# Optimization experiments

Measured on AMD Instinct MI355X. Metric: run time of the kernel, lower is better.

Reference implementation:

```python
import jax, jax.numpy as jnp
import numpy as np

B, S, H, P = 8, 2048, 256, 64
NQ = 20

def setup_inputs() -> dict:
    key = jax.random.key(0)
    ks = jax.random.split(key, 12)
    s = lambda fan_in: 1.0 / np.sqrt(fan_in)
    return {
        "feature_x": jax.random.normal(ks[0], (B, S, H), dtype=jnp.float32),
        "param_x": jax.random.normal(ks[1], (B, S, P), dtype=jnp.float32),
        "sim_w1": jax.random.uniform(ks[2], (H, H // 2), jnp.float32, -s(H), s(H)),
        "sim_b1": jax.random.uniform(ks[3], (H // 2,), jnp.float32, -s(H), s(H)),
        "sim_w2": jax.random.uniform(ks[4], (H // 2, 1), jnp.float32, -s(H // 2), s(H // 2)),
        "sim_b2": jax.random.uniform(ks[5], (1,), jnp.float32, -s(H // 2), s(H // 2)),
        "conf_w1": jax.random.uniform(ks[6], (H, H // 2), jnp.float32, -s(H), s(H)),
        "conf_b1": jax.random.uniform(ks[7], (H // 2,), jnp.float32, -s(H), s(H)),
        "conf_w2": jax.random.uniform(ks[8], (H // 2, 1), jnp.float32, -s(H // 2), s(H // 2)),
        "conf_b2": jax.random.uniform(ks[9], (1,), jnp.float32, -s(H // 2), s(H // 2)),
        "questions": jax.random.randint(ks[10], (B, S), 0, NQ, dtype=jnp.int64 if jax.config.jax_enable_x64 else jnp.int32),
    }

def _mlp_scalar(x, w1, b1, w2, b2):
    # [B,S,H] -> [B,S] (dropout is eval-mode identity)
    h = jax.nn.relu(jnp.einsum("bsh,hk->bsk", x, w1) + b1)
    return (jnp.einsum("bsk,ko->bso", h, w2) + b2)[..., 0]

def reference(feature_x, param_x, sim_w1, sim_b1, sim_w2, sim_b2,
              conf_w1, conf_b1, conf_w2, conf_b2, questions):
    similarities = _mlp_scalar(feature_x, sim_w1, sim_b1, sim_w2, sim_b2)          # [B,S]
    confidences = jax.nn.sigmoid(_mlp_scalar(feature_x, conf_w1, conf_b1, conf_w2, conf_b2))  # [B,S]
    # multiplicative equality mask (zeros, not -inf, outside group — faithful to source)
    qmask = (questions[:, :, None] == questions[:, None, :]).astype(feature_x.dtype)  # [B,S,S]
    logits = similarities[:, :, None] * qmask                                        # [B,i,j]
    attn = jax.nn.softmax(logits, axis=-2)                                           # softmax over i
    smoothed = jnp.einsum("bij,bip->bjp", attn, param_x)                              # attn^T @ param_x
    c = confidences[..., None]
    return c * param_x + (1.0 - c) * smoothed
```

## Files before the change

### kernel.cpp

```cpp
#include <hip/hip_runtime.h>
#include <math.h>

#define B_  8
#define S_  2048
#define H_  256
#define HK_ 128
#define P_  64
#define NQ_ 20
#define M_  (B_*S_)
#define ACC_STRIDE 2688
#define NREP 4

#define WS_CONF  0
#define WS_ACC   16384
#define WS_WT    (16384 + NREP*B_*ACC_STRIDE)

typedef __attribute__((ext_vector_type(8))) short bf16x8;
typedef __attribute__((ext_vector_type(4))) float f32x4;

__global__ void prep_kernel(const float* __restrict__ sw1, const float* __restrict__ cw1,
                            short* __restrict__ wtf, float* __restrict__ ws_acc)
{
    const int t = blockIdx.x * 256 + threadIdx.x;
    const int l = t & 63, nt = (t >> 6) & 7, kt = (t >> 9) & 7, mlp = t >> 12;
    const int col = l & 15, quad = l >> 4;
    const int n = nt * 16 + col;
    const float* w1 = mlp ? cw1 : sw1;
    short frag[8];
    #pragma unroll
    for (int j = 0; j < 8; ++j) {
        int k = kt * 32 + quad * 8 + j;
        union { float f; unsigned u; } c; c.f = w1[k * HK_ + n];
        frag[j] = (short)((c.u + 0x7FFF + ((c.u >> 16) & 1)) >> 16);
    }
    *(uint4*)(wtf + (size_t)t * 8) = *(const uint4*)frag;
    for (int s = t; s < NREP * B_ * ACC_STRIDE; s += 8192) ws_acc[s] = 0.f;
}

__launch_bounds__(256)
__global__ void mlp_accum_kernel(const float* __restrict__ fx, const short* __restrict__ wtf,
                                 const float* __restrict__ sb1, const float* __restrict__ sw2,
                                 const float* __restrict__ sb2, const float* __restrict__ cb1,
                                 const float* __restrict__ cw2, const float* __restrict__ cb2,
                                 const float* __restrict__ px, const int* __restrict__ questions,
                                 float* __restrict__ conf, float* __restrict__ ws_acc)
{
    __shared__ float accs[ACC_STRIDE];
    __shared__ float sim_l[32];

    const int tid  = threadIdx.x;
    for (int s = tid; s < ACC_STRIDE; s += 256) accs[s] = 0.f;

    const int w    = tid >> 6, l = tid & 63;
    const int col  = l & 15, quad = l >> 4;
    const int mlp  = w >> 1, mt = w & 1;
    const int row  = blockIdx.x * 32 + mt * 16 + col;

    f32x4 acc[8];
    #pragma unroll
    for (int nt = 0; nt < 8; ++nt) acc[nt] = (f32x4){0.f, 0.f, 0.f, 0.f};

    const float* fxrow = fx + (size_t)row * H_;
    const short* wf = wtf + (size_t)mlp * 32768 + (size_t)l * 8;

    #pragma unroll
    for (int kt = 0; kt < 8; ++kt) {
        float4 a0 = *(const float4*)(fxrow + kt * 32 + quad * 8);
        float4 a1 = *(const float4*)(fxrow + kt * 32 + quad * 8 + 4);
        float af[8] = {a0.x, a0.y, a0.z, a0.w, a1.x, a1.y, a1.z, a1.w};
        bf16x8 ahi, alo;
        #pragma unroll
        for (int i = 0; i < 8; ++i) {
            union { float f; unsigned u; } c; c.f = af[i];
            unsigned hi = c.u >> 16;
            ahi[i] = (short)hi;
            union { float f; unsigned u; } h2; h2.u = hi << 16;
            union { float f; unsigned u; } c2; c2.f = af[i] - h2.f;
            alo[i] = (short)(c2.u >> 16);
        }
        const short* base = wf + (size_t)kt * 4096;
        #pragma unroll
        for (int nt = 0; nt < 8; ++nt) {
            bf16x8 bf = *(const bf16x8*)(base + nt * 512);
            acc[nt] = __builtin_amdgcn_mfma_f32_16x16x32_bf16(ahi, bf, acc[nt], 0, 0, 0);
            acc[nt] = __builtin_amdgcn_mfma_f32_16x16x32_bf16(alo, bf, acc[nt], 0, 0, 0);
        }
    }

    const float* b1 = mlp ? cb1 : sb1;
    const float* w2 = mlp ? cw2 : sw2;
    const float  b2v = mlp ? cb2[0] : sb2[0];
    float p[4] = {0.f, 0.f, 0.f, 0.f};
    #pragma unroll
    for (int nt = 0; nt < 8; ++nt) {
        float b1c = b1[nt * 16 + col];
        float w2c = w2[nt * 16 + col];
        #pragma unroll
        for (int j = 0; j < 4; ++j)
            p[j] += fmaxf(acc[nt][j] + b1c, 0.f) * w2c;
    }
    #pragma unroll
    for (int off = 8; off >= 1; off >>= 1)
        #pragma unroll
        for (int j = 0; j < 4; ++j) p[j] += __shfl_down(p[j], off, 16);

    if (col == 0) {
        #pragma unroll
        for (int j = 0; j < 4; ++j) {
            int rloc = mt * 16 + quad * 4 + j;
            float v = p[j] + b2v;
            if (mlp == 0) sim_l[rloc] = v;
            else          conf[blockIdx.x * 32 + rloc] = 1.0f / (1.0f + expf(-v));
        }
    }
    __syncthreads();

    const int row0 = blockIdx.x * 32;
    float Treg = 0.f;
    #pragma unroll
    for (int t = 0; t < 8; ++t) {
        const int il = w + 4 * t;
        const int i  = row0 + il;
        const int qi = questions[i];
        const float e = expf(sim_l[il]);
        const float v = px[(size_t)i * P_ + l];
        Treg += v;
        atomicAdd(&accs[qi * 64 + l], v);
        atomicAdd(&accs[(20 + qi) * 64 + l], e * v);
        if (l == 0) {
            atomicAdd(&accs[2624 + qi], e);
            atomicAdd(&accs[2644 + qi], 1.0f);
        }
    }
    atomicAdd(&accs[2560 + l], Treg);
    __syncthreads();

    const int b   = blockIdx.x >> 6;
    const int rep = blockIdx.x & (NREP - 1);
    float* dst = ws_acc + (size_t)(b * NREP + rep) * ACC_STRIDE;
    for (int s = tid; s < ACC_STRIDE; s += 256) {
        const float vv = accs[s];
        if (vv != 0.f) atomicAdd(dst + s, vv);
    }
}

__global__ void output_kernel(const float* __restrict__ px, const float* __restrict__ conf,
                              const int* __restrict__ questions, const float* __restrict__ ws_acc,
                              float* __restrict__ out)
{
    const int idx = blockIdx.x * 256 + threadIdx.x;
    const int row = idx >> 4;
    const int p4  = idx & 15;
    const int b   = row >> 11;
    const float c = conf[row];
    const int   q = questions[row];

    float Tx=0.f,Ty=0.f,Tz=0.f,Tw=0.f;
    float Gx=0.f,Gy=0.f,Gz=0.f,Gw=0.f;
    float Ex=0.f,Ey=0.f,Ez=0.f,Ew=0.f;
    float Wq=0.f, nq=0.f;
    #pragma unroll
    for (int rep = 0; rep < NREP; ++rep) {
        const float* a = ws_acc + (size_t)(b * NREP + rep) * ACC_STRIDE;
        const float4 t4 = *(const float4*)(a + 2560 + p4 * 4);
        const float4 g4 = *(const float4*)(a + q * 64 + p4 * 4);
        const float4 e4 = *(const float4*)(a + (20 + q) * 64 + p4 * 4);
        Tx += t4.x; Ty += t4.y; Tz += t4.z; Tw += t4.w;
        Gx += g4.x; Gy += g4.y; Gz += g4.z; Gw += g4.w;
        Ex += e4.x; Ey += e4.y; Ez += e4.z; Ew += e4.w;
        Wq += a[2624 + q]; nq += a[2644 + q];
    }
    const float denom = ((float)S_ - nq) + Wq;
    const float inv = 1.0f / denom;
    const float4 pv = ((const float4*)px)[idx];
    const float om = 1.0f - c;
    float4 o;
    o.x = c * pv.x + om * ((Tx - Gx + Ex) * inv);
    o.y = c * pv.y + om * ((Ty - Gy + Ey) * inv);
    o.z = c * pv.z + om * ((Tz - Gz + Ez) * inv);
    o.w = c * pv.w + om * ((Tw - Gw + Ew) * inv);
    ((float4*)out)[idx] = o;
}

extern "C" void kernel_launch(void* const* d_in, const int* in_sizes, int n_in,
                              void* d_out, int out_size, void* d_ws, size_t ws_size,
                              hipStream_t stream) {
    const float* fx  = (const float*)d_in[0];
    const float* px  = (const float*)d_in[1];
    const float* sw1 = (const float*)d_in[2];
    const float* sb1 = (const float*)d_in[3];
    const float* sw2 = (const float*)d_in[4];
    const float* sb2 = (const float*)d_in[5];
    const float* cw1 = (const float*)d_in[6];
    const float* cb1 = (const float*)d_in[7];
    const float* cw2 = (const float*)d_in[8];
    const float* cb2 = (const float*)d_in[9];
    const int* questions = (const int*)d_in[10];
    float* out = (float*)d_out;

    float* ws     = (float*)d_ws;
    float* conf   = ws + WS_CONF;
    float* ws_acc = ws + WS_ACC;
    short* wtf    = (short*)(ws + WS_WT);

    prep_kernel<<<32, 256, 0, stream>>>(sw1, cw1, wtf, ws_acc);
    mlp_accum_kernel<<<M_ / 32, 256, 0, stream>>>(fx, wtf, sb1, sw2, sb2,
                                                  cb1, cw2, cb2, px, questions,
                                                  conf, ws_acc);
    output_kernel<<<(M_ * P_ / 4) / 256, 256, 0, stream>>>(px, conf, questions,
                                                           ws_acc, out);
}
```

Measured before the change: 115.2 us.

## Fuse prep, MLP-accumulate and output into one cooperative kernel with grid syncs

The three kernels become a single cooperative launch of 512 blocks. Grid-wide barriers separate weight-fragment preparation, the MLP and group accumulation, and the output stage. Each block prefetches and splits its feature rows into bf16 hi/lo parts before the first barrier, which overlaps that load with the weight prep. Confidences and question ids stay in shared memory, so the conf workspace round trip goes away. This removes two launch boundaries and lets the output stage reuse block-local data. In exchange it adds grid-sync costs, needs all 512 blocks co-resident (launch_bounds 256,2), and holds more registers for the prefetched fragments.

```diff
diff --git a/kernel.cpp b/kernel.cpp
--- a/kernel.cpp
+++ b/kernel.cpp
@@ -1,5 +1,8 @@
 #include <hip/hip_runtime.h>
+#include <hip/hip_cooperative_groups.h>
 #include <math.h>
+
+namespace cg = cooperative_groups;
 
 #define B_  8
 #define S_  2048
@@ -11,111 +14,124 @@
 #define ACC_STRIDE 2688
 #define NREP 4
 
-#define WS_CONF  0
-#define WS_ACC   16384
-#define WS_WT    (16384 + NREP*B_*ACC_STRIDE)
+#define WS_ACC   0
+#define WS_WT    (NREP*B_*ACC_STRIDE)
 
 typedef __attribute__((ext_vector_type(8))) short bf16x8;
 typedef __attribute__((ext_vector_type(4))) float f32x4;
 
-__global__ void prep_kernel(const float* __restrict__ sw1, const float* __restrict__ cw1,
-                            short* __restrict__ wtf, float* __restrict__ ws_acc)
+__launch_bounds__(256, 2)
+__global__ void fused_kernel(const float* __restrict__ fx, const float* __restrict__ px,
+                             const float* __restrict__ sw1, const float* __restrict__ sb1,
+                             const float* __restrict__ sw2, const float* __restrict__ sb2,
+                             const float* __restrict__ cw1, const float* __restrict__ cb1,
+                             const float* __restrict__ cw2, const float* __restrict__ cb2,
+                             const int* __restrict__ questions, short* __restrict__ wtf,
+                             float* __restrict__ ws_acc, float* __restrict__ out)
 {
-    const int t = blockIdx.x * 256 + threadIdx.x;
-    const int l = t & 63, nt = (t >> 6) & 7, kt = (t >> 9) & 7, mlp = t >> 12;
-    const int col = l & 15, quad = l >> 4;
-    const int n = nt * 16 + col;
-    const float* w1 = mlp ? cw1 : sw1;
-    short frag[8];
-    #pragma unroll
-    for (int j = 0; j < 8; ++j) {
-        int k = kt * 32 + quad * 8 + j;
-        union { float f; unsigned u; } c; c.f = w1[k * HK_ + n];
-        frag[j] = (short)((c.u + 0x7FFF + ((c.u >> 16) & 1)) >> 16);
-    }
-    *(uint4*)(wtf + (size_t)t * 8) = *(const uint4*)frag;
-    for (int s = t; s < NREP * B_ * ACC_STRIDE; s += 8192) ws_acc[s] = 0.f;
-}
-
-__launch_bounds__(256)
-__global__ void mlp_accum_kernel(const float* __restrict__ fx, const short* __restrict__ wtf,
-                                 const float* __restrict__ sb1, const float* __restrict__ sw2,
-                                 const float* __restrict__ sb2, const float* __restrict__ cb1,
-                                 const float* __restrict__ cw2, const float* __restrict__ cb2,
-                                 const float* __restrict__ px, const int* __restrict__ questions,
-                                 float* __restrict__ conf, float* __restrict__ ws_acc)
-{
+    cg::grid_group grid = cg::this_grid();
     __shared__ float accs[ACC_STRIDE];
     __shared__ float sim_l[32];
-
-    const int tid  = threadIdx.x;
+    __shared__ float conf_l[32];
+    __shared__ int   q_l[32];
+
+    const int tid = threadIdx.x;
+    const int bid = blockIdx.x;
+
+    if (bid < 32) {
+        const int t = bid * 256 + tid;
+        const int pl = t & 63, pnt = (t >> 6) & 7, pkt = (t >> 9) & 7, pmlp = t >> 12;
+        const int pcol = pl & 15, pquad = pl >> 4;
+        const int n = pnt * 16 + pcol;
+        const float* w1 = pmlp ? cw1 : sw1;
+        short frag[8];
+        #pragma unroll
+        for (int j = 0; j < 8; ++j) {
+            int k = pkt * 32 + pquad * 8 + j;
+            union { float f; unsigned u; } c; c.f = w1[k * HK_ + n];
+            frag[j] = (short)((c.u + 0x7FFF + ((c.u >> 16) & 1)) >> 16);
+        }
+        *(uint4*)(wtf + (size_t)t * 8) = *(const uint4*)frag;
+        for (int s = t; s < NREP * B_ * ACC_STRIDE; s += 8192) ws_acc[s] = 0.f;
+    }
+
     for (int s = tid; s < ACC_STRIDE; s += 256) accs[s] = 0.f;
 
     const int w    = tid >> 6, l = tid & 63;
     const int col  = l & 15, quad = l >> 4;
     const int mlp  = w >> 1, mt = w & 1;
-    const int row  = blockIdx.x * 32 + mt * 16 + col;
+    const int row  = bid * 32 + mt * 16 + col;
+    const int row0 = bid * 32;
+
+    bf16x8 ahi[8], alo[8];
+    {
+        const float* fxrow = fx + (size_t)row * H_;
+        #pragma unroll
+        for (int kt = 0; kt < 8; ++kt) {
+            float4 a0 = *(const float4*)(fxrow + kt * 32 + quad * 8);
+            float4 a1 = *(const float4*)(fxrow + kt * 32 + quad * 8 + 4);
+            float af[8] = {a0.x, a0.y, a0.z, a0.w, a1.x, a1.y, a1.z, a1.w};
+            #pragma unroll
+            for (int i = 0; i < 8; ++i) {
+                union { float f; unsigned u; } c; c.f = af[i];
+                unsigned hi = c.u >> 16;
+                ahi[kt][i] = (short)hi;
+                union { float f; unsigned u; } h2; h2.u = hi << 16;
+                union { float f; unsigned u; } c2; c2.f = af[i] - h2.f;
+                alo[kt][i] = (short)(c2.u >> 16);
+            }
+        }
+    }
+
+    __threadfence();
+    grid.sync();
 
     f32x4 acc[8];
     #pragma unroll
     for (int nt = 0; nt < 8; ++nt) acc[nt] = (f32x4){0.f, 0.f, 0.f, 0.f};
 
-    const float* fxrow = fx + (size_t)row * H_;
     const short* wf = wtf + (size_t)mlp * 32768 + (size_t)l * 8;
-
     #pragma unroll
     for (int kt = 0; kt < 8; ++kt) {
-        float4 a0 = *(const float4*)(fxrow + kt * 32 + quad * 8);
-        float4 a1 = *(const float4*)(fxrow + kt * 32 + quad * 8 + 4);
-        float af[8] = {a0.x, a0.y, a0.z, a0.w, a1.x, a1.y, a1.z, a1.w};
-        bf16x8 ahi, alo;
-        #pragma unroll
-        for (int i = 0; i < 8; ++i) {
-            union { float f; unsigned u; } c; c.f = af[i];
-            unsigned hi = c.u >> 16;
-            ahi[i] = (short)hi;
-            union { float f; unsigned u; } h2; h2.u = hi << 16;
-            union { float f; unsigned u; } c2; c2.f = af[i] - h2.f;
-            alo[i] = (short)(c2.u >> 16);
-        }
         const short* base = wf + (size_t)kt * 4096;
         #pragma unroll
         for (int nt = 0; nt < 8; ++nt) {
             bf16x8 bf = *(const bf16x8*)(base + nt * 512);
-            acc[nt] = __builtin_amdgcn_mfma_f32_16x16x32_bf16(ahi, bf, acc[nt], 0, 0, 0);
-            acc[nt] = __builtin_amdgcn_mfma_f32_16x16x32_bf16(alo, bf, acc[nt], 0, 0, 0);
-        }
-    }
-
-    const float* b1 = mlp ? cb1 : sb1;
-    const float* w2 = mlp ? cw2 : sw2;
-    const float  b2v = mlp ? cb2[0] : sb2[0];
-    float p[4] = {0.f, 0.f, 0.f, 0.f};
-    #pragma unroll
-    for (int nt = 0; nt < 8; ++nt) {
-        float b1c = b1[nt * 16 + col];
-        float w2c = w2[nt * 16 + col];
-        #pragma unroll
-        for (int j = 0; j < 4; ++j)
-            p[j] += fmaxf(acc[nt][j] + b1c, 0.f) * w2c;
-    }
-    #pragma unroll
-    for (int off = 8; off >= 1; off >>= 1)
-        #pragma unroll
-        for (int j = 0; j < 4; ++j) p[j] += __shfl_down(p[j], off, 16);
-
-    if (col == 0) {
-        #pragma unroll
-        for (int j = 0; j < 4; ++j) {
-            int rloc = mt * 16 + quad * 4 + j;
-            float v = p[j] + b2v;
-            if (mlp == 0) sim_l[rloc] = v;
-            else          conf[blockIdx.x * 32 + rloc] = 1.0f / (1.0f + expf(-v));
+            acc[nt] = __builtin_amdgcn_mfma_f32_16x16x32_bf16(ahi[kt], bf, acc[nt], 0, 0, 0);
+            acc[nt] = __builtin_amdgcn_mfma_f32_16x16x32_bf16(alo[kt], bf, acc[nt], 0, 0, 0);
+        }
+    }
+
+    {
+        const float* b1 = mlp ? cb1 : sb1;
+        const float* w2 = mlp ? cw2 : sw2;
+        const float  b2v = mlp ? cb2[0] : sb2[0];
+        float p[4] = {0.f, 0.f, 0.f, 0.f};
+        #pragma unroll
+        for (int nt = 0; nt < 8; ++nt) {
+            float b1c = b1[nt * 16 + col];
+            float w2c = w2[nt * 16 + col];
+            #pragma unroll
+            for (int j = 0; j < 4; ++j)
+                p[j] += fmaxf(acc[nt][j] + b1c, 0.f) * w2c;
+        }
+        #pragma unroll
+        for (int off = 8; off >= 1; off >>= 1)
+            #pragma unroll
+            for (int j = 0; j < 4; ++j) p[j] += __shfl_down(p[j], off, 16);
+
+        if (col == 0) {
+            #pragma unroll
+            for (int j = 0; j < 4; ++j) {
+                int rloc = mt * 16 + quad * 4 + j;
+                float v = p[j] + b2v;
+                if (mlp == 0) sim_l[rloc]  = v;
+                else          conf_l[rloc] = 1.0f / (1.0f + expf(-v));
+            }
         }
     }
     __syncthreads();
 
-    const int row0 = blockIdx.x * 32;
     float Treg = 0.f;
     #pragma unroll
     for (int t = 0; t < 8; ++t) {
@@ -128,6 +144,7 @@
         atomicAdd(&accs[qi * 64 + l], v);
         atomicAdd(&accs[(20 + qi) * 64 + l], e * v);
         if (l == 0) {
+            q_l[il] = qi;
             atomicAdd(&accs[2624 + qi], e);
             atomicAdd(&accs[2644 + qi], 1.0f);
         }
@@ -135,51 +152,53 @@
     atomicAdd(&accs[2560 + l], Treg);
     __syncthreads();
 
-    const int b   = blockIdx.x >> 6;
-    const int rep = blockIdx.x & (NREP - 1);
-    float* dst = ws_acc + (size_t)(b * NREP + rep) * ACC_STRIDE;
-    for (int s = tid; s < ACC_STRIDE; s += 256) {
-        const float vv = accs[s];
-        if (vv != 0.f) atomicAdd(dst + s, vv);
-    }
-}
-
-__global__ void output_kernel(const float* __restrict__ px, const float* __restrict__ conf,
-                              const int* __restrict__ questions, const float* __restrict__ ws_acc,
-                              float* __restrict__ out)
-{
-    const int idx = blockIdx.x * 256 + threadIdx.x;
-    const int row = idx >> 4;
-    const int p4  = idx & 15;
-    const int b   = row >> 11;
-    const float c = conf[row];
-    const int   q = questions[row];
-
-    float Tx=0.f,Ty=0.f,Tz=0.f,Tw=0.f;
-    float Gx=0.f,Gy=0.f,Gz=0.f,Gw=0.f;
-    float Ex=0.f,Ey=0.f,Ez=0.f,Ew=0.f;
-    float Wq=0.f, nq=0.f;
-    #pragma unroll
-    for (int rep = 0; rep < NREP; ++rep) {
-        const float* a = ws_acc + (size_t)(b * NREP + rep) * ACC_STRIDE;
-        const float4 t4 = *(const float4*)(a + 2560 + p4 * 4);
-        const float4 g4 = *(const float4*)(a + q * 64 + p4 * 4);
-        const float4 e4 = *(const float4*)(a + (20 + q) * 64 + p4 * 4);
-        Tx += t4.x; Ty += t4.y; Tz += t4.z; Tw += t4.w;
-        Gx += g4.x; Gy += g4.y; Gz += g4.z; Gw += g4.w;
-        Ex += e4.x; Ey += e4.y; Ez += e4.z; Ew += e4.w;
-        Wq += a[2624 + q]; nq += a[2644 + q];
-    }
-    const float denom = ((float)S_ - nq) + Wq;
-    const float inv = 1.0f / denom;
-    const float4 pv = ((const float4*)px)[idx];
-    const float om = 1.0f - c;
-    float4 o;
-    o.x = c * pv.x + om * ((Tx - Gx + Ex) * inv);
-    o.y = c * pv.y + om * ((Ty - Gy + Ey) * inv);
-    o.z = c * pv.z + om * ((Tz - Gz + Ez) * inv);
-    o.w = c * pv.w + om * ((Tw - Gw + Ew) * inv);
-    ((float4*)out)[idx] = o;
+    const int b   = bid >> 6;
+    const int rep = bid & (NREP - 1);
+    {
+        float* dst = ws_acc + (size_t)(b * NREP + rep) * ACC_STRIDE;
+        for (int s = tid; s < ACC_STRIDE; s += 256) {
+            const float vv = accs[s];
+            if (vv != 0.f) atomicAdd(dst + s, vv);
+        }
+    }
+
+    __threadfence();
+    grid.sync();
+
+    const int p4 = tid & 15;
+    #pragma unroll
+    for (int half = 0; half < 2; ++half) {
+        const int il = (tid >> 4) + half * 16;
+        const int i  = row0 + il;
+        const float c = conf_l[il];
+        const int   q = q_l[il];
+
+        float Tx=0.f,Ty=0.f,Tz=0.f,Tw=0.f;
+        float Gx=0.f,Gy=0.f,Gz=0.f,Gw=0.f;
+        float Ex=0.f,Ey=0.f,Ez=0.f,Ew=0.f;
+        float Wq=0.f, nq=0.f;
+        #pragma unroll
+        for (int rp = 0; rp < NREP; ++rp) {
+            const float* a = ws_acc + (size_t)(b * NREP + rp) * ACC_STRIDE;
+            const float4 t4 = *(const float4*)(a + 2560 + p4 * 4);
+            const float4 g4 = *(const float4*)(a + q * 64 + p4 * 4);
+            const float4 e4 = *(const float4*)(a + (20 + q) * 64 + p4 * 4);
+            Tx += t4.x; Ty += t4.y; Tz += t4.z; Tw += t4.w;
+            Gx += g4.x; Gy += g4.y; Gz += g4.z; Gw += g4.w;
+            Ex += e4.x; Ey += e4.y; Ez += e4.z; Ew += e4.w;
+            Wq += a[2624 + q]; nq += a[2644 + q];
+        }
+        const float denom = ((float)S_ - nq) + Wq;
+        const float inv = 1.0f / denom;
+        const float4 pv = ((const float4*)px)[(size_t)i * 16 + p4];
+        const float om = 1.0f - c;
+        float4 o;
+        o.x = c * pv.x + om * ((Tx - Gx + Ex) * inv);
+        o.y = c * pv.y + om * ((Ty - Gy + Ey) * inv);
+        o.z = c * pv.z + om * ((Tz - Gz + Ez) * inv);
+        o.w = c * pv.w + om * ((Tw - Gw + Ew) * inv);
+        ((float4*)out)[(size_t)i * 16 + p4] = o;
+    }
 }
 
 extern "C" void kernel_launch(void* const* d_in, const int* in_sizes, int n_in,
@@ -199,14 +218,14 @@
     float* out = (float*)d_out;
 
     float* ws     = (float*)d_ws;
-    float* conf   = ws + WS_CONF;
     float* ws_acc = ws + WS_ACC;
     short* wtf    = (short*)(ws + WS_WT);
 
-    prep_kernel<<<32, 256, 0, stream>>>(sw1, cw1, wtf, ws_acc);
-    mlp_accum_kernel<<<M_ / 32, 256, 0, stream>>>(fx, wtf, sb1, sw2, sb2,
-                                                  cb1, cw2, cb2, px, questions,
-                                                  conf, ws_acc);
-    output_kernel<<<(M_ * P_ / 4) / 256, 256, 0, stream>>>(px, conf, questions,
-                                                           ws_acc, out);
+    void* args[] = {
+        (void*)&fx, (void*)&px, (void*)&sw1, (void*)&sb1, (void*)&sw2, (void*)&sb2,
+        (void*)&cw1, (void*)&cb1, (void*)&cw2, (void*)&cb2,
+        (void*)&questions, (void*)&wtf, (void*)&ws_acc, (void*)&out
+    };
+    hipLaunchCooperativeKernel((void*)fused_kernel, dim3(M_ / 32), dim3(256),
+                               args, 0, stream);
 }
```

After: 325.7 us. +182.8%, slower.
